# Optimization experiments

Hardware: AMD Instinct MI355X
Metric: run time of the kernel (lower is better)

## Reference

```python
import jax, jax.numpy as jnp
import numpy as np

B, L = 8, 1024
VOCAB, D_ENC, D_MAIN = 260, 128, 256
N_ENC, N_MAIN, N_DEC, N_HEADS = 3, 6, 3, 4
N_RATIO = 6.0  # 1/target_ratio
NEG = jnp.float32(-1e9)


def setup_inputs() -> dict:
    key = jax.random.key(0)
    kc = iter(jax.random.split(key, 40))
    def nrm(shape, std):
        return jax.random.normal(next(kc), shape, jnp.float32) * std
    inp = {'byte_ids': jax.random.randint(next(kc), (B, L), 0, VOCAB)}
    inp['embed'] = nrm((VOCAB, D_ENC), D_ENC ** -0.5)
    eye = jnp.eye(D_ENC, dtype=jnp.float32)
    inp['wq'] = eye + nrm((D_ENC, D_ENC), 0.02)  # init is identity in the torch module
    inp['wk'] = eye + nrm((D_ENC, D_ENC), 0.02)
    inp['proj_up'] = nrm((D_MAIN, D_ENC), D_ENC ** -0.5)
    inp['proj_down'] = nrm((D_ENC, D_MAIN), 1e-3)
    inp['norm_w'] = jnp.ones((D_ENC,), jnp.float32)
    inp['norm_b'] = jnp.zeros((D_ENC,), jnp.float32)
    for pre, n, d in [('enc', N_ENC, D_ENC), ('main', N_MAIN, D_MAIN), ('dec', N_DEC, D_ENC)]:
        inp[pre + '_ln1_w'] = jnp.ones((n, d), jnp.float32)
        inp[pre + '_ln1_b'] = jnp.zeros((n, d), jnp.float32)
        inp[pre + '_qkv'] = nrm((n, 3 * d, d), d ** -0.5)   # MHA in_proj (3D, D)
        inp[pre + '_wo'] = nrm((n, d, d), d ** -0.5)        # MHA out_proj
        inp[pre + '_ln2_w'] = jnp.ones((n, d), jnp.float32)
        inp[pre + '_ln2_b'] = jnp.zeros((n, d), jnp.float32)
        inp[pre + '_w1'] = nrm((n, 2 * d, d), d ** -0.5)    # mlp_mult = 2
        inp[pre + '_w2'] = nrm((n, d, 2 * d), (2 * d) ** -0.5)
    return inp


def _ln(x, w, b):
    mu = jnp.mean(x, axis=-1, keepdims=True)
    var = jnp.mean((x - mu) ** 2, axis=-1, keepdims=True)
    return (x - mu) * jax.lax.rsqrt(var + 1e-5) * w + b


def _mha(x, wqkv, wo, bias):
    Bb, S, D = x.shape
    dh = D // N_HEADS
    q, k, v = jnp.split(x @ wqkv.T, 3, axis=-1)
    q = q.reshape(Bb, S, N_HEADS, dh)
    k = k.reshape(Bb, S, N_HEADS, dh)
    v = v.reshape(Bb, S, N_HEADS, dh)
    scores = jnp.einsum('bqhd,bkhd->bhqk', q, k) * (dh ** -0.5) + bias
    attn = jax.nn.softmax(scores, axis=-1)
    out = jnp.einsum('bhqk,bkhd->bqhd', attn, v).reshape(Bb, S, D)
    return out @ wo.T


def _block(x, stack, i, bias):
    ln1w, ln1b, qkv, wo, ln2w, ln2b, w1, w2 = (a[i] for a in stack)
    x = x + _mha(_ln(x, ln1w, ln1b), qkv, wo, bias)
    h = _ln(x, ln2w, ln2b)
    return x + jax.nn.gelu(h @ w1.T, approximate=False) @ w2.T


def _downsample(x, b_hard):
    # scatter boundary tokens to the front of a padded (B, S, D) buffer
    Bb, S, D = x.shape
    idx = jnp.cumsum(b_hard, axis=1).astype(jnp.int32) - 1
    dest = jnp.where(b_hard > 0.5, idx, S)  # S is out-of-range -> dropped
    def sc(xb, db):
        return jnp.zeros((S, D), xb.dtype).at[db].set(xb, mode='drop')
    out = jax.vmap(sc)(x, dest)
    counts = jnp.sum(b_hard, axis=1).astype(jnp.int32)
    mask = jnp.arange(S)[None, :] < counts[:, None]
    return out, mask


def _forward(byte_ids, embed, wq, wk,
             enc_ln1_w, enc_ln1_b, enc_qkv, enc_wo, enc_ln2_w, enc_ln2_b, enc_w1, enc_w2,
             proj_up,
             main_ln1_w, main_ln1_b, main_qkv, main_wo, main_ln2_w, main_ln2_b, main_w1, main_w2,
             proj_down,
             dec_ln1_w, dec_ln1_b, dec_qkv, dec_wo, dec_ln2_w, dec_ln2_b, dec_w1, dec_w2,
             norm_w, norm_b):
    causal = jnp.where(jnp.triu(jnp.ones((L, L), bool), 1), NEG, jnp.float32(0.0))[None, None]
    x = embed[byte_ids]  # (B, L, D_ENC)
    enc_p = (enc_ln1_w, enc_ln1_b, enc_qkv, enc_wo, enc_ln2_w, enc_ln2_b, enc_w1, enc_w2)
    for i in range(N_ENC):
        x = _block(x, enc_p, i, causal)

    # --- dynamic chunking (routing + ratio loss) ---
    def l2n(t):
        return t / jnp.maximum(jnp.linalg.norm(t, axis=-1, keepdims=True), 1e-12)
    q = l2n(x @ wq.T)
    k = l2n(x @ wk.T)
    k_prev = jnp.pad(k[:, :-1], ((0, 0), (1, 0), (0, 0)))
    cos = jnp.sum(q * k_prev, axis=-1)
    p = jnp.clip(0.5 * (1.0 - cos), 0.0, 1.0)
    p = jnp.concatenate([jnp.ones_like(p[:, :1]), p[:, 1:]], axis=1)
    b_hard = (p >= 0.5).astype(jnp.float32)
    N = N_RATIO
    F_act = jnp.mean(b_hard)
    G_act = jnp.mean(p)
    ratio_loss = N / (N - 1.0) * ((N - 1.0) * F_act * G_act + (1.0 - F_act) * (1.0 - G_act))
    compressed, comp_mask = _downsample(x, b_hard)
    p_comp = _downsample(p[..., None], b_hard)[0][..., 0]

    # --- main stack on compressed sequence (padded to L, masked) ---
    z = compressed @ proj_up.T
    main_bias = causal + jnp.where(comp_mask, jnp.float32(0.0), NEG)[:, None, None, :]
    main_p = (main_ln1_w, main_ln1_b, main_qkv, main_wo, main_ln2_w, main_ln2_b, main_w1, main_w2)
    for i in range(N_MAIN):
        z = _block(z, main_p, i, main_bias)
    z = z @ proj_down.T  # (B, L, D_ENC)

    # --- chunk-level EMA (parallel linear-recurrence scan) + gather + STE ---
    p_c = jnp.clip(p_comp, 1e-4, 1.0 - 1e-4)
    a = (1.0 - p_c).at[:, 0].set(0.0)[..., None]          # z_bar[0] = z[0]
    bv = (p_c[..., None] * z).at[:, :1].set(z[:, :1])
    def comb(lhs, rhs):
        al, bl = lhs
        ar, br = rhs
        return (al * ar, ar * bl + br)
    z_bar = jax.lax.associative_scan(comb, (a, bv), axis=1)[1]
    chunk_idx = jnp.clip(jnp.cumsum(b_hard, axis=1).astype(jnp.int32) - 1, 0, None)
    z_up = jnp.take_along_axis(z_bar, jnp.broadcast_to(chunk_idx[:, :, None], z_bar.shape), axis=1)
    c = b_hard * p + (1.0 - b_hard) * (1.0 - p)
    c_ste = c + jax.lax.stop_gradient(1.0 - c)
    x = x + c_ste[..., None] * z_up

    dec_p = (dec_ln1_w, dec_ln1_b, dec_qkv, dec_wo, dec_ln2_w, dec_ln2_b, dec_w1, dec_w2)
    for i in range(N_DEC):
        x = _block(x, dec_p, i, causal)
    x = _ln(x, norm_w, norm_b)
    logits = x @ embed.T  # tied head
    return logits, ratio_loss


def reference(byte_ids, embed, wq, wk,
              enc_ln1_w, enc_ln1_b, enc_qkv, enc_wo, enc_ln2_w, enc_ln2_b, enc_w1, enc_w2,
              proj_up,
              main_ln1_w, main_ln1_b, main_qkv, main_wo, main_ln2_w, main_ln2_b, main_w1, main_w2,
              proj_down,
              dec_ln1_w, dec_ln1_b, dec_qkv, dec_wo, dec_ln2_w, dec_ln2_b, dec_w1, dec_w2,
              norm_w, norm_b):
    return _forward(byte_ids, embed, wq, wk,
                    enc_ln1_w, enc_ln1_b, enc_qkv, enc_wo, enc_ln2_w, enc_ln2_b, enc_w1, enc_w2,
                    proj_up,
                    main_ln1_w, main_ln1_b, main_qkv, main_wo, main_ln2_w, main_ln2_b, main_w1, main_w2,
                    proj_down,
                    dec_ln1_w, dec_ln1_b, dec_qkv, dec_wo, dec_ln2_w, dec_ln2_b, dec_w1, dec_w2,
                    norm_w, norm_b)
```

## Files before the change

### kernel.cpp

```cpp
#include <hip/hip_runtime.h>
#include <hip/hip_bf16.h>

#define B_ 8
#define L_ 1024
#define BL (B_*L_)
#define DENC 128
#define DMAIN 256
#define VOCAB 260
#define NHEADS 4

typedef __hip_bfloat16 bf16;
typedef _Float16 f16;
typedef f16 half8 __attribute__((ext_vector_type(8)));
typedef f16 half4 __attribute__((ext_vector_type(4)));
typedef f16 half2v __attribute__((ext_vector_type(2)));
typedef float f32x4 __attribute__((ext_vector_type(4)));

__global__ __launch_bounds__(64) void k_detect(const void* __restrict__ emb, int* __restrict__ flag){
    int lane = threadIdx.x;
    const unsigned short* u = (const unsigned short*)emb;
    int bad = 0;
    #pragma unroll
    for (int j = 0; j < 4; j++){
        unsigned short h = u[lane + 64*j];
        bf16 t = *(const bf16*)&h;
        float v = __bfloat162float(t);
        if (!(fabsf(v) < 1e4f)) bad++;
    }
    #pragma unroll
    for (int o = 32; o >= 1; o >>= 1) bad += __shfl_xor(bad, o);
    if (lane == 0) flag[0] = (bad == 0) ? 1 : 0;
}

struct CvtArgs {
    const void* src[31];
    unsigned offs[32];
};
__global__ void k_cvt_all(CvtArgs a, float* __restrict__ dst, f16* __restrict__ dst16,
                          int total, const int* __restrict__ flag){
    int isbf = flag[0];
    for (int i = blockIdx.x*256 + threadIdx.x; i < total; i += gridDim.x*256){
        int lo = 0, hi = 30;
        while (lo < hi){ int mid = (lo+hi+1)>>1; if (a.offs[mid] <= (unsigned)i) lo = mid; else hi = mid-1; }
        int j = i - (int)a.offs[lo];
        float v = isbf ? __bfloat162float(((const bf16*)a.src[lo])[j])
                       : ((const float*)a.src[lo])[j];
        dst[i] = v;
        dst16[i] = (f16)v;
    }
}

__global__ void k_embed(const int* __restrict__ ids, const float* __restrict__ emb, float* __restrict__ x){
    int i = blockIdx.x*256 + threadIdx.x;
    int row = i >> 7, d = i & 127;
    x[i] = emb[ids[row]*DENC + d];
}

template<int D>
__global__ __launch_bounds__(256) void k_ln16(const float* __restrict__ x, const float* __restrict__ w,
                                              const float* __restrict__ b, f16* __restrict__ y){
    int row = blockIdx.x*4 + (threadIdx.x >> 6);
    int lane = threadIdx.x & 63;
    const float* xr = x + (size_t)row*D;
    float v[D/64];
    float s = 0.f;
    #pragma unroll
    for (int j=0;j<D/64;j++){ v[j] = xr[lane + j*64]; s += v[j]; }
    #pragma unroll
    for (int o=32;o>=1;o>>=1) s += __shfl_xor(s,o);
    float mu = s / (float)D;
    float s2 = 0.f;
    #pragma unroll
    for (int j=0;j<D/64;j++){ float dd = v[j]-mu; s2 += dd*dd; }
    #pragma unroll
    for (int o=32;o>=1;o>>=1) s2 += __shfl_xor(s2,o);
    float inv = rsqrtf(s2/(float)D + 1e-5f);
    f16* yr = y + (size_t)row*D;
    #pragma unroll
    for (int j=0;j<D/64;j++){
        int d = lane + j*64;
        yr[d] = (f16)((v[j]-mu)*inv*w[d] + b[d]);
    }
}

#define GBM 64
#define GBN 64
#define GBK 32
__global__ __launch_bounds__(256) void k_gemm2(const float* __restrict__ A, const float* __restrict__ Wq,
        const float* __restrict__ Wk, float* __restrict__ Cq, float* __restrict__ Ck, int K)
{
    __shared__ float As[GBK][GBM+4];
    __shared__ float Ws[GBK][GBN+4];
    int tid = threadIdx.x;
    int bm = blockIdx.y * GBM;
    int bn = blockIdx.x * GBN;
    int tx = tid & 15, ty = tid >> 4;
    float acc[4][4] = {};
    for (int k0 = 0; k0 < K; k0 += GBK){
        #pragma unroll
        for (int i = tid; i < GBM*GBK; i += 256){
            int m = i >> 5, kk = i & 31;
            As[kk][m] = A[(size_t)(bm+m)*K + k0 + kk];
        }
        #pragma unroll
        for (int i = tid; i < GBN*GBK; i += 256){
            int n = i >> 5, kk = i & 31;
            int gn = bn + n;
            const float* W = (gn < 128) ? Wq : Wk;
            int wr = gn & 127;
            Ws[kk][n] = W[(size_t)wr*K + k0 + kk];
        }
        __syncthreads();
        #pragma unroll
        for (int kk = 0; kk < GBK; kk++){
            float a0[4], w0[4];
            *(float4*)a0 = *(const float4*)&As[kk][ty*4];
            *(float4*)w0 = *(const float4*)&Ws[kk][tx*4];
            #pragma unroll
            for (int i=0;i<4;i++)
                #pragma unroll
                for (int j=0;j<4;j++) acc[i][j] += a0[i]*w0[j];
        }
        __syncthreads();
    }
    #pragma unroll
    for (int i=0;i<4;i++){
        int m = bm + ty*4 + i;
        #pragma unroll
        for (int j=0;j<4;j++){
            int n = bn + tx*4 + j;
            float* C = (n < 128) ? Cq : Ck;
            C[(size_t)m*128 + (n & 127)] = acc[i][j];
        }
    }
}

template<int K>
__global__ __launch_bounds__(256) void k_hgemm(const f16* __restrict__ A, const f16* __restrict__ W,
        const float* __restrict__ R, float* __restrict__ C, f16* __restrict__ C16,
        void* __restrict__ OutRaw, const int* __restrict__ flag, int N, int mode,
        f16* __restrict__ Qd, f16* __restrict__ Kd, f16* __restrict__ Vd,
        int dShift, int dhShift)
{
    __shared__ half8 As[4][64];
    __shared__ half8 Ws[4][64];
    int tid = threadIdx.x;
    int wave = tid >> 6, lane = tid & 63;
    int wr = wave >> 1, wc = wave & 1;
    int quad = lane >> 4, l15 = lane & 15;
    int bm = blockIdx.y * 64, bn = blockIdx.x * 64;

    f32x4 acc[2][2] = {};
    int srow = tid >> 2, sc8 = tid & 3;
    const f16* ap0 = A + (size_t)(bm + srow)*K + sc8*8;
    int gn = bn + srow;
    const f16* wp0 = W + (size_t)gn*K + sc8*8;
    bool wok = (gn < N);

    for (int k0 = 0; k0 < K; k0 += 32){
        __syncthreads();
        As[sc8][srow] = *(const half8*)(ap0 + k0);
        Ws[sc8][srow] = wok ? *(const half8*)(wp0 + k0) : (half8)(f16)0.f;
        __syncthreads();
        half8 af[2], wf[2];
        af[0] = As[quad][wr*32 + l15];
        af[1] = As[quad][wr*32 + 16 + l15];
        wf[0] = Ws[quad][wc*32 + l15];
        wf[1] = Ws[quad][wc*32 + 16 + l15];
        #pragma unroll
        for (int i=0;i<2;i++)
            #pragma unroll
            for (int j=0;j<2;j++)
                acc[i][j] = __builtin_amdgcn_mfma_f32_16x16x32_f16(af[i], wf[j], acc[i][j], 0, 0, 0);
    }

    #pragma unroll
    for (int j=0;j<2;j++){
        int n = bn + wc*32 + j*16 + l15;
        if (n >= N) continue;
        #pragma unroll
        for (int i=0;i<2;i++){
            #pragma unroll
            for (int r=0;r<4;r++){
                int m = bm + wr*32 + i*16 + quad*4 + r;
                float v = acc[i][j][r];
                if (mode == 5){
                    int which = n >> dShift;
                    int rem = n & ((1<<dShift)-1);
                    int hh = rem >> dhShift;
                    int dd = rem & ((1<<dhShift)-1);
                    int bb = m >> 10, tt = m & 1023;
                    int Hn = 1 << (dShift - dhShift);
                    f16* dst = (which==0) ? Qd : ((which==1) ? Kd : Vd);
                    if (which == 2)
                        dst[((((size_t)bb*Hn + hh) << dhShift) + dd)*L_ + tt] = (f16)v;
                    else
                        dst[((((size_t)bb*Hn + hh)*L_ + tt) << dhShift) + dd] = (f16)v;
                    continue;
                }
                size_t off = (size_t)m*N + n;
                if (mode == 1){ C[off] = v + R[off]; }
                else if (mode == 2){
                    v = 0.5f*v*(1.0f + erff(v*0.70710678118654752f));
                    C16[off] = (f16)v;
                } else if (mode == 3){
                    if (flag[0]) ((bf16*)OutRaw)[off] = __float2bfloat16(v);
                    else         ((float*)OutRaw)[off] = v;
                } else C[off] = v;
            }
        }
    }
}

template<int K>
__global__ __launch_bounds__(256) void k_lngemm(const float* __restrict__ A, const f16* __restrict__ W,
        const float* __restrict__ lnw, const float* __restrict__ lnb, int doLN,
        float* __restrict__ C, void* __restrict__ OutRaw,
        const int* __restrict__ flag, int N, int mode)
{
    constexpr int SA = K + 8;
    constexpr int RPT = K/64;
    __shared__ f16 sA[64*SA];
    int tid = threadIdx.x;
    int wave = tid >> 6, lane = tid & 63;
    int wr = wave >> 1, wc = wave & 1;
    int quad = lane >> 4, l15 = lane & 15;
    int bm = blockIdx.y * 64, bn = blockIdx.x * 64;

    float wv_[RPT], bv_[RPT];
    #pragma unroll
    for (int j=0;j<RPT;j++){
        int d = lane*RPT + j;
        wv_[j] = doLN ? lnw[d] : 1.f;
        bv_[j] = doLN ? lnb[d] : 0.f;
    }
    for (int rr=0; rr<16; rr++){
        int row = wave*16 + rr;
        const float* xr = A + (size_t)(bm+row)*K + lane*RPT;
        float v[RPT];
        if (RPT==2){ float2 t = *(const float2*)xr; v[0]=t.x; v[1]=t.y; }
        else       { float4 t = *(const float4*)xr; v[0]=t.x; v[1]=t.y; v[2]=t.z; v[3]=t.w; }
        float mu = 0.f, inv = 1.f;
        if (doLN){
            float s=0.f;
            #pragma unroll
            for (int j=0;j<RPT;j++) s += v[j];
            #pragma unroll
            for (int o=32;o>=1;o>>=1) s += __shfl_xor(s,o);
            mu = s / (float)K;
            float s2=0.f;
            #pragma unroll
            for (int j=0;j<RPT;j++){ float dd=v[j]-mu; s2+=dd*dd; }
            #pragma unroll
            for (int o=32;o>=1;o>>=1) s2 += __shfl_xor(s2,o);
            inv = rsqrtf(s2/(float)K + 1e-5f);
        }
        if (RPT==2){
            half2v h;
            h[0]=(f16)((v[0]-mu)*inv*wv_[0]+bv_[0]);
            h[1]=(f16)((v[1]-mu)*inv*wv_[1]+bv_[1]);
            *(half2v*)&sA[row*SA + lane*2] = h;
        } else {
            half4 h;
            #pragma unroll
            for (int j=0;j<4;j++) h[j]=(f16)((v[j]-mu)*inv*wv_[j]+bv_[j]);
            *(half4*)&sA[row*SA + lane*4] = h;
        }
    }
    __syncthreads();

    f32x4 acc[2][2] = {};
    int n0 = bn + wc*32 + l15;
    bool ok0 = n0 < N, ok1 = (n0+16) < N;
    const f16* w0p = W + (size_t)n0*K + quad*8;
    const f16* w1p = W + (size_t)(n0+16)*K + quad*8;
    #pragma unroll 4
    for (int k0=0;k0<K;k0+=32){
        half8 af[2], wf[2];
        af[0] = *(const half8*)&sA[(wr*32 + l15)*SA + k0 + quad*8];
        af[1] = *(const half8*)&sA[(wr*32 + 16 + l15)*SA + k0 + quad*8];
        wf[0] = ok0 ? *(const half8*)(w0p + k0) : (half8)(f16)0.f;
        wf[1] = ok1 ? *(const half8*)(w1p + k0) : (half8)(f16)0.f;
        #pragma unroll
        for (int i=0;i<2;i++)
            #pragma unroll
            for (int j=0;j<2;j++)
                acc[i][j] = __builtin_amdgcn_mfma_f32_16x16x32_f16(af[i], wf[j], acc[i][j], 0, 0, 0);
    }

    #pragma unroll
    for (int j=0;j<2;j++){
        int n = bn + wc*32 + j*16 + l15;
        if (n >= N) continue;
        #pragma unroll
        for (int i=0;i<2;i++){
            #pragma unroll
            for (int r=0;r<4;r++){
                int m = bm + wr*32 + i*16 + quad*4 + r;
                float v = acc[i][j][r];
                size_t off = (size_t)m*N + n;
                if (mode == 3){
                    if (flag[0]) ((bf16*)OutRaw)[off] = __float2bfloat16(v);
                    else         ((float*)OutRaw)[off] = v;
                } else C[off] = v;
            }
        }
    }
}

template<int DH>
__global__ __launch_bounds__(256) void k_mflash(const f16* __restrict__ Qh, const f16* __restrict__ Kh,
        const f16* __restrict__ Vt, f16* __restrict__ out, const int* __restrict__ counts,
        float scale)
{
    constexpr int BQ = 64, BK = 64;
    constexpr int RS = DH + 8;
    constexpr int PS = BK + 8;
    __shared__ f16 sQ[BQ*RS];
    __shared__ f16 sK[BK*RS];
    __shared__ f16 sVt[DH*PS];
    __shared__ f16 sP[BQ*PS];

    int x = blockIdx.x, b = x >> 2, h = x & 3;
    int yy = blockIdx.y;
    int qt = (yy < 8) ? yy : 23 - yy;
    int q0 = qt * BQ;
    int tid = threadIdx.x;
    int wv = tid >> 6, lane = tid & 63;
    int quad = lane >> 4, l15 = lane & 15;

    const f16* Qb = Qh + (size_t)x*L_*DH;
    const f16* Kb = Kh + (size_t)x*L_*DH;
    const f16* Vb = Vt + (size_t)x*DH*L_;
    int kcap = counts ? counts[b] : L_;
    int klen = min(kcap, q0 + BQ);

    for (int i = tid; i < BQ*DH/8; i += 256){
        int r = (8*i)/DH, c = (8*i)%DH;
        *(half8*)&sQ[r*RS + c] = *(const half8*)&Qb[(size_t)(q0+r)*DH + c];
    }

    float m[4], l[4];
    #pragma unroll
    for (int r=0;r<4;r++){ m[r] = -1e30f; l[r] = 0.f; }
    f32x4 accO[DH/16] = {};

    for (int k0 = 0; k0 < klen; k0 += BK){
        __syncthreads();
        for (int i = tid; i < BK*DH/8; i += 256){
            int r = (8*i)/DH, c = (8*i)%DH;
            *(half8*)&sK[r*RS + c] = *(const half8*)&Kb[(size_t)(k0+r)*DH + c];
        }
        for (int i = tid; i < DH*BK/8; i += 256){
            int r = (8*i)/BK, c = (8*i)%BK;
            *(half8*)&sVt[r*PS + c] = *(const half8*)&Vb[(size_t)r*L_ + k0 + c];
        }
        __syncthreads();

        half8 af[DH/32];
        #pragma unroll
        for (int ds=0; ds<DH/32; ds++)
            af[ds] = *(const half8*)&sQ[(16*wv + l15)*RS + quad*8 + 32*ds];
        f32x4 accS[4] = {};
        #pragma unroll
        for (int t=0;t<4;t++){
            #pragma unroll
            for (int ds=0; ds<DH/32; ds++){
                half8 bf = *(const half8*)&sK[(16*t + l15)*RS + quad*8 + 32*ds];
                accS[t] = __builtin_amdgcn_mfma_f32_16x16x32_f16(af[ds], bf, accS[t], 0, 0, 0);
            }
        }

        #pragma unroll
        for (int r=0;r<4;r++){
            int qrow = q0 + 16*wv + quad*4 + r;
            float sv[4];
            #pragma unroll
            for (int t=0;t<4;t++){
                float v = accS[t][r]*scale;
                int kp = k0 + 16*t + l15;
                if (kp > qrow || kp >= kcap) v = -1e30f;
                sv[t] = v;
            }
            float rm = fmaxf(fmaxf(sv[0],sv[1]), fmaxf(sv[2],sv[3]));
            rm = fmaxf(rm, __shfl_xor(rm, 1));
            rm = fmaxf(rm, __shfl_xor(rm, 2));
            rm = fmaxf(rm, __shfl_xor(rm, 4));
            rm = fmaxf(rm, __shfl_xor(rm, 8));
            float mn = fmaxf(m[r], rm);
            float al = __expf(m[r] - mn);
            float p0 = __expf(sv[0]-mn), p1 = __expf(sv[1]-mn);
            float p2 = __expf(sv[2]-mn), p3 = __expf(sv[3]-mn);
            float rs = p0+p1+p2+p3;
            rs += __shfl_xor(rs, 1);
            rs += __shfl_xor(rs, 2);
            rs += __shfl_xor(rs, 4);
            rs += __shfl_xor(rs, 8);
            l[r] = l[r]*al + rs;
            m[r] = mn;
            #pragma unroll
            for (int dt=0; dt<DH/16; dt++) accO[dt][r] *= al;
            int prow = 16*wv + quad*4 + r;
            sP[prow*PS + 16*0 + l15] = (f16)p0;
            sP[prow*PS + 16*1 + l15] = (f16)p1;
            sP[prow*PS + 16*2 + l15] = (f16)p2;
            sP[prow*PS + 16*3 + l15] = (f16)p3;
        }

        half8 pf[2];
        #pragma unroll
        for (int ks=0; ks<2; ks++)
            pf[ks] = *(const half8*)&sP[(16*wv + l15)*PS + quad*8 + 32*ks];
        #pragma unroll
        for (int dt=0; dt<DH/16; dt++){
            #pragma unroll
            for (int ks=0; ks<2; ks++){
                half8 bv = *(const half8*)&sVt[(16*dt + l15)*PS + quad*8 + 32*ks];
                accO[dt] = __builtin_amdgcn_mfma_f32_16x16x32_f16(pf[ks], bv, accO[dt], 0, 0, 0);
            }
        }
    }

    #pragma unroll
    for (int r=0;r<4;r++){
        float inv = 1.0f / l[r];
        int qrow = q0 + 16*wv + quad*4 + r;
        #pragma unroll
        for (int dt=0; dt<DH/16; dt++){
            int d = 16*dt + l15;
            out[((size_t)b*L_ + qrow)*(NHEADS*DH) + h*DH + d] = (f16)(accO[dt][r]*inv);
        }
    }
}

__global__ __launch_bounds__(64) void k_router(const float* __restrict__ Q, const float* __restrict__ Kr,
        float* __restrict__ p, float* __restrict__ bh)
{
    int idx = blockIdx.x;
    int t = idx & (L_-1);
    int lane = threadIdx.x;
    float pv;
    if (t == 0){ pv = 1.0f; }
    else {
        const float* qr = Q  + (size_t)idx*DENC;
        const float* kr = Kr + (size_t)(idx-1)*DENC;
        float qq=0.f, kk=0.f, qk=0.f;
        #pragma unroll
        for (int j=0;j<2;j++){
            float qv = qr[lane + j*64], kv = kr[lane + j*64];
            qq += qv*qv; kk += kv*kv; qk += qv*kv;
        }
        #pragma unroll
        for (int o=32;o>=1;o>>=1){ qq += __shfl_xor(qq,o); kk += __shfl_xor(kk,o); qk += __shfl_xor(qk,o); }
        float cosv = qk / (fmaxf(sqrtf(qq),1e-12f)*fmaxf(sqrtf(kk),1e-12f));
        pv = 0.5f*(1.0f - cosv);
        pv = fminf(fmaxf(pv, 0.0f), 1.0f);
    }
    if (lane == 0){ p[idx] = pv; bh[idx] = (pv >= 0.5f) ? 1.0f : 0.0f; }
}

__global__ __launch_bounds__(64) void k_seq(const float* __restrict__ bh, int* __restrict__ cidx,
                      int* __restrict__ src, int* __restrict__ counts, float* __restrict__ acc){
    int b = blockIdx.x;
    int lane = threadIdx.x;
    if (b == 0 && lane < 8) acc[lane] = 0.f;
    int base = b*L_ + lane*16;
    int h[16];
    int cnt = 0;
    #pragma unroll
    for (int j=0;j<16;j++){ h[j] = bh[base+j] > 0.5f; cnt += h[j]; }
    int inc = cnt;
    #pragma unroll
    for (int o=1;o<64;o<<=1){ int nb = __shfl_up(inc, o); if (lane >= o) inc += nb; }
    int run = inc - cnt;
    #pragma unroll
    for (int j=0;j<16;j++){
        run += h[j];
        int ci = run - 1; if (ci < 0) ci = 0;
        cidx[base+j] = ci;
        if (h[j]) src[b*L_ + run-1] = lane*16 + j;
    }
    if (lane == 63) counts[b] = inc;
}

__global__ __launch_bounds__(128) void k_scatter2(const float* __restrict__ x, const float* __restrict__ p,
        const int* __restrict__ src, const int* __restrict__ counts,
        f16* __restrict__ comp, float* __restrict__ pcomp)
{
    int s = blockIdx.x & (L_-1), b = blockIdx.x >> 10, d = threadIdx.x;
    int cnt = counts[b];
    f16* crow = comp + ((size_t)b*L_ + s)*DENC;
    if (s < cnt){
        int t = src[b*L_ + s];
        crow[d] = (f16)x[((size_t)b*L_ + t)*DENC + d];
        if (d == 0) pcomp[b*L_ + s] = p[b*L_ + t];
    } else {
        crow[d] = (f16)0.f;
        if (d == 0) pcomp[b*L_ + s] = 0.f;
    }
}

__global__ __launch_bounds__(256) void k_reduce(const float* __restrict__ p, const float* __restrict__ bh,
                                                float* __restrict__ acc){
    __shared__ float sp[256], sb[256];
    int tid = threadIdx.x;
    float s1=0.f, s2=0.f;
    for (int i = blockIdx.x*256 + tid; i < BL; i += gridDim.x*256){ s1 += p[i]; s2 += bh[i]; }
    sp[tid]=s1; sb[tid]=s2; __syncthreads();
    for (int o=128;o>=1;o>>=1){ if (tid<o){ sp[tid]+=sp[tid+o]; sb[tid]+=sb[tid+o]; } __syncthreads(); }
    if (tid==0){ atomicAdd(&acc[0], sp[0]); atomicAdd(&acc[1], sb[0]); }
}

__global__ __launch_bounds__(256) void k_ema2(const float* __restrict__ z, const float* __restrict__ pcomp,
                                              float* __restrict__ zbar){
    __shared__ float sp[L_];
    int blk = blockIdx.x;
    int b = blk >> 5;
    int tid = threadIdx.x, wv = tid >> 6, lane = tid & 63;
    int d = ((blk & 31) << 2) + wv;
    for (int i = tid; i < L_; i += 256){
        float pc = pcomp[b*L_ + i];
        sp[i] = fminf(fmaxf(pc, 1e-4f), 1.0f - 1e-4f);
    }
    __syncthreads();
    const float* zb = z + ((size_t)b*L_)*DENC + d;
    int t0 = lane*16;
    float zv[16];
    #pragma unroll
    for (int i=0;i<16;i++) zv[i] = zb[(size_t)(t0+i)*DENC];
    float A = 1.f, Bv = 0.f;
    #pragma unroll
    for (int i=0;i<16;i++){
        int t = t0 + i;
        float pc = sp[t];
        float a  = (t==0) ? 0.f : (1.f - pc);
        float bb = (t==0) ? zv[i] : pc*zv[i];
        A = a*A;
        Bv = a*Bv + bb;
    }
    #pragma unroll
    for (int off=1; off<64; off<<=1){
        float Ap = __shfl_up(A, off);
        float Bp = __shfl_up(Bv, off);
        if (lane >= off){ Bv = A*Bp + Bv; A = A*Ap; }
    }
    float sin_ = __shfl_up(Bv, 1);
    if (lane == 0) sin_ = 0.f;
    float s = sin_;
    float* ob = zbar + ((size_t)b*L_)*DENC + d;
    #pragma unroll
    for (int i=0;i<16;i++){
        int t = t0 + i;
        float pc = sp[t];
        float a  = (t==0) ? 0.f : (1.f - pc);
        float bb = (t==0) ? zv[i] : pc*zv[i];
        s = a*s + bb;
        ob[(size_t)t*DENC] = s;
    }
}

__global__ void k_combine(float* __restrict__ x, const float* __restrict__ zbar, const int* __restrict__ cidx){
    int i = blockIdx.x*256 + threadIdx.x;
    int row = i >> 7, d = i & 127;
    int b = row >> 10;
    int ci = cidx[row];
    x[i] += zbar[((size_t)b*L_ + ci)*DENC + d];
}

__global__ void k_loss(const float* __restrict__ acc, void* __restrict__ out, const int* __restrict__ flag){
    float G = acc[0] / (float)BL;
    float F = acc[1] / (float)BL;
    float ratio = 1.2f*(5.0f*F*G + (1.0f-F)*(1.0f-G));
    if (flag[0]) ((bf16*)out)[(size_t)BL*VOCAB] = __float2bfloat16(ratio);
    else         ((float*)out)[(size_t)BL*VOCAB] = ratio;
}

extern "C" void kernel_launch(void* const* d_in, const int* in_sizes, int n_in,
                              void* d_out, int out_size, void* d_ws, size_t ws_size,
                              hipStream_t stream) {
    (void)out_size; (void)ws_size;
    const int* byte_ids = (const int*)d_in[0];

    float* ws = (float*)d_ws;
    size_t off = 0;
    int* FLAG = (int*)ws; off += 16;
    float* W32 = ws + off;

    k_detect<<<1, 64, 0, stream>>>(d_in[1], FLAG);

    CvtArgs ca;
    const float* w32[32];
    unsigned woff = 0;
    for (int i = 1; i < n_in && i < 32; i++){
        w32[i] = W32 + woff;
        ca.src[i-1] = d_in[i];
        ca.offs[i-1] = woff;
        woff += (unsigned)in_sizes[i];
    }
    ca.offs[31] = woff;
    off += woff;
    f16* W16h = (f16*)(ws + off); off += (woff+1)/2;
    const f16* w16[32];
    for (int i = 1; i < n_in && i < 32; i++) w16[i] = W16h + ca.offs[i-1];
    k_cvt_all<<<2048, 256, 0, stream>>>(ca, W32, W16h, (int)woff, FLAG);

    const float* embed    = w32[1];
    const float* wq       = w32[2];
    const float* wk       = w32[3];
    const float* norm_w   = w32[6];
    const float* norm_b   = w32[7];

    float* X    = ws + off; off += (size_t)BL*DENC;
    float* QKVf = ws + off; off += (size_t)BL*3*DMAIN;
    float* ATTf = ws + off; off += (size_t)BL*DMAIN;
    float* Hf   = ws + off; off += (size_t)BL*2*DMAIN;
    float* LNf  = ws + off; off += (size_t)BL*DMAIN;
    float* Z    = ws + off; off += (size_t)BL*DMAIN;
    float* COMPf= ws + off; off += (size_t)BL*DENC;
    float* P    = ws + off; off += BL;
    float* BH   = ws + off; off += BL;
    float* PCOMP= ws + off; off += BL;
    float* ACC  = ws + off; off += 8;
    int* CIDX   = (int*)(ws + off); off += BL;
    int* SRC    = (int*)(ws + off); off += BL;
    int* COUNTS = (int*)(ws + off); off += 64;

    f16* QKV16 = (f16*)QKVf;
    f16* ATT16 = (f16*)ATTf;
    f16* H16   = (f16*)Hf;
    f16* LN16  = (f16*)LNf;
    f16* COMP16= (f16*)COMPf;
    float* Qr  = ATTf;
    float* Kr  = Hf;
    float* ZDN = QKVf;
    float* ZBAR= QKVf + (size_t)BL*DENC;

    auto hgemm = [&](int K, const f16* A, const f16* W, const float* R, float* C, f16* C16,
                     void* Ob, int N, int mode, f16* Qd, f16* Kd, f16* Vd, int dS, int dhS){
        dim3 g((N+63)/64, BL/64);
        if (K == 128)      k_hgemm<128><<<g, 256, 0, stream>>>(A, W, R, C, C16, Ob, FLAG, N, mode, Qd, Kd, Vd, dS, dhS);
        else if (K == 256) k_hgemm<256><<<g, 256, 0, stream>>>(A, W, R, C, C16, Ob, FLAG, N, mode, Qd, Kd, Vd, dS, dhS);
        else               k_hgemm<512><<<g, 256, 0, stream>>>(A, W, R, C, C16, Ob, FLAG, N, mode, Qd, Kd, Vd, dS, dhS);
    };

    auto block128 = [&](float* Xs, const float* l1w, const float* l1b, const f16* qkvw, const f16* wo,
                        const float* l2w, const float* l2b, const f16* w1, const f16* w2){
        k_ln16<128><<<BL/4,256,0,stream>>>(Xs, l1w, l1b, LN16);
        hgemm(128, LN16, qkvw, nullptr, nullptr, nullptr, nullptr, 3*DENC, 5,
              QKV16, QKV16 + (size_t)BL*DENC, QKV16 + (size_t)2*BL*DENC, 7, 5);
        k_mflash<32><<<dim3(B_*NHEADS,16),256,0,stream>>>(QKV16, QKV16 + (size_t)BL*DENC,
                                                          QKV16 + (size_t)2*BL*DENC,
                                                          ATT16, nullptr, 0.17677669529663687f);
        hgemm(128, ATT16, wo, Xs, Xs, nullptr, nullptr, DENC, 1, nullptr, nullptr, nullptr, 0, 0);
        k_ln16<128><<<BL/4,256,0,stream>>>(Xs, l2w, l2b, LN16);
        hgemm(128, LN16, w1, nullptr, nullptr, H16, nullptr, 2*DENC, 2, nullptr, nullptr, nullptr, 0, 0);
        hgemm(256, H16, w2, Xs, Xs, nullptr, nullptr, DENC, 1, nullptr, nullptr, nullptr, 0, 0);
    };
    auto block_main = [&](float* Xs, const float* l1w, const float* l1b, const f16* qkvw, const f16* wo,
                          const float* l2w, const float* l2b, const f16* w1, const f16* w2){
        k_ln16<256><<<BL/4,256,0,stream>>>(Xs, l1w, l1b, LN16);
        hgemm(256, LN16, qkvw, nullptr, nullptr, nullptr, nullptr, 3*DMAIN, 5,
              QKV16, QKV16 + (size_t)BL*DMAIN, QKV16 + (size_t)2*BL*DMAIN, 8, 6);
        k_mflash<64><<<dim3(B_*NHEADS,16),256,0,stream>>>(QKV16, QKV16 + (size_t)BL*DMAIN,
                                                          QKV16 + (size_t)2*BL*DMAIN,
                                                          ATT16, COUNTS, 0.125f);
        hgemm(256, ATT16, wo, Xs, Xs, nullptr, nullptr, DMAIN, 1, nullptr, nullptr, nullptr, 0, 0);
        k_ln16<256><<<BL/4,256,0,stream>>>(Xs, l2w, l2b, LN16);
        hgemm(256, LN16, w1, nullptr, nullptr, H16, nullptr, 2*DMAIN, 2, nullptr, nullptr, nullptr, 0, 0);
        hgemm(512, H16, w2, Xs, Xs, nullptr, nullptr, DMAIN, 1, nullptr, nullptr, nullptr, 0, 0);
    };

    k_embed<<<BL*DENC/256, 256, 0, stream>>>(byte_ids, embed, X);
    for (int i = 0; i < 3; i++)
        block128(X, w32[8] + i*DENC, w32[9] + i*DENC, w16[10] + (size_t)i*3*DENC*DENC,
                 w16[11] + (size_t)i*DENC*DENC, w32[12] + i*DENC, w32[13] + i*DENC,
                 w16[14] + (size_t)i*2*DENC*DENC, w16[15] + (size_t)i*2*DENC*DENC);

    k_gemm2<<<dim3(4, BL/64), 256, 0, stream>>>(X, wq, wk, Qr, Kr, DENC);
    k_router<<<BL, 64, 0, stream>>>(Qr, Kr, P, BH);
    k_seq<<<B_, 64, 0, stream>>>(BH, CIDX, SRC, COUNTS, ACC);
    k_scatter2<<<BL, 128, 0, stream>>>(X, P, SRC, COUNTS, COMP16, PCOMP);
    k_reduce<<<8, 256, 0, stream>>>(P, BH, ACC);

    hgemm(128, COMP16, w16[4], nullptr, Z, nullptr, nullptr, DMAIN, 0, nullptr, nullptr, nullptr, 0, 0);
    for (int i = 0; i < 6; i++)
        block_main(Z, w32[16] + i*DMAIN, w32[17] + i*DMAIN, w16[18] + (size_t)i*3*DMAIN*DMAIN,
                   w16[19] + (size_t)i*DMAIN*DMAIN, w32[20] + i*DMAIN, w32[21] + i*DMAIN,
                   w16[22] + (size_t)i*2*DMAIN*DMAIN, w16[23] + (size_t)i*2*DMAIN*DMAIN);
    k_lngemm<256><<<dim3(2, BL/64), 256, 0, stream>>>(Z, w16[5], nullptr, nullptr, 0,
                                                      ZDN, nullptr, FLAG, DENC, 0);

    k_ema2<<<256, 256, 0, stream>>>(ZDN, PCOMP, ZBAR);
    k_combine<<<BL*DENC/256, 256, 0, stream>>>(X, ZBAR, CIDX);

    for (int i = 0; i < 3; i++)
        block128(X, w32[24] + i*DENC, w32[25] + i*DENC, w16[26] + (size_t)i*3*DENC*DENC,
                 w16[27] + (size_t)i*DENC*DENC, w32[28] + i*DENC, w32[29] + i*DENC,
                 w16[30] + (size_t)i*2*DENC*DENC, w16[31] + (size_t)i*2*DENC*DENC);

    k_lngemm<128><<<dim3(5, BL/64), 256, 0, stream>>>(X, w16[1], norm_w, norm_b, 1,
                                                      nullptr, d_out, FLAG, VOCAB, 3);
    k_loss<<<1,1,0,stream>>>(ACC, d_out, FLAG);
}
```

Baseline: 1.216 ms.

## Add 128-row hgemm tile with K=64 steps and fold reduction into k_seq

The f16 MFMA GEMM now loads a 64-wide K slice per iteration, issuing two MFMA k-steps per barrier pair instead of one. A BM=128 variant, where each wave owns 32 rows across all 64 columns, is used for the wide QKV and main-stack W1 projections. The separate k_reduce kernel is removed: k_seq now reduces p and the boundary count per sequence with atomics, and zeroing of the accumulator moves into k_router. This cuts the number of syncs per K, raises reuse of the W tile and drops one launch, at the cost of more LDS, more registers and fewer blocks for the wide GEMMs.

```diff
diff --git a/kernel.cpp b/kernel.cpp
--- a/kernel.cpp
+++ b/kernel.cpp
@@ -135,54 +135,65 @@
     }
 }
 
-template<int K>
+template<int K, int BM>
 __global__ __launch_bounds__(256) void k_hgemm(const f16* __restrict__ A, const f16* __restrict__ W,
         const float* __restrict__ R, float* __restrict__ C, f16* __restrict__ C16,
         void* __restrict__ OutRaw, const int* __restrict__ flag, int N, int mode,
         f16* __restrict__ Qd, f16* __restrict__ Kd, f16* __restrict__ Vd,
         int dShift, int dhShift)
 {
-    __shared__ half8 As[4][64];
-    __shared__ half8 Ws[4][64];
+    constexpr int NJ = (BM == 128) ? 4 : 2;
+    __shared__ half8 As[BM*8];
+    __shared__ half8 Ws[64*8];
     int tid = threadIdx.x;
     int wave = tid >> 6, lane = tid & 63;
-    int wr = wave >> 1, wc = wave & 1;
     int quad = lane >> 4, l15 = lane & 15;
-    int bm = blockIdx.y * 64, bn = blockIdx.x * 64;
-
-    f32x4 acc[2][2] = {};
-    int srow = tid >> 2, sc8 = tid & 3;
-    const f16* ap0 = A + (size_t)(bm + srow)*K + sc8*8;
-    int gn = bn + srow;
-    const f16* wp0 = W + (size_t)gn*K + sc8*8;
-    bool wok = (gn < N);
-
-    for (int k0 = 0; k0 < K; k0 += 32){
+    int bm = blockIdx.y * BM, bn = blockIdx.x * 64;
+    int mrow0 = (BM == 128) ? wave*32 : (wave>>1)*32;
+    int ncol0 = (BM == 128) ? 0 : (wave&1)*32;
+
+    f32x4 acc[2][NJ] = {};
+
+    for (int k0 = 0; k0 < K; k0 += 64){
         __syncthreads();
-        As[sc8][srow] = *(const half8*)(ap0 + k0);
-        Ws[sc8][srow] = wok ? *(const half8*)(wp0 + k0) : (half8)(f16)0.f;
+        #pragma unroll
+        for (int s = 0; s < BM/32; s++){
+            int slot = s*256 + tid;
+            int row = slot >> 3, col = slot & 7;
+            As[slot] = *(const half8*)(A + (size_t)(bm+row)*K + k0 + col*8);
+        }
+        #pragma unroll
+        for (int s = 0; s < 2; s++){
+            int slot = s*256 + tid;
+            int row = slot >> 3, col = slot & 7;
+            int gn = bn + row;
+            Ws[slot] = (gn < N) ? *(const half8*)(W + (size_t)gn*K + k0 + col*8) : (half8)(f16)0.f;
+        }
         __syncthreads();
-        half8 af[2], wf[2];
-        af[0] = As[quad][wr*32 + l15];
-        af[1] = As[quad][wr*32 + 16 + l15];
-        wf[0] = Ws[quad][wc*32 + l15];
-        wf[1] = Ws[quad][wc*32 + 16 + l15];
-        #pragma unroll
-        for (int i=0;i<2;i++)
-            #pragma unroll
-            for (int j=0;j<2;j++)
-                acc[i][j] = __builtin_amdgcn_mfma_f32_16x16x32_f16(af[i], wf[j], acc[i][j], 0, 0, 0);
-    }
-
-    #pragma unroll
-    for (int j=0;j<2;j++){
-        int n = bn + wc*32 + j*16 + l15;
+        #pragma unroll
+        for (int ks = 0; ks < 2; ks++){
+            half8 af[2], wf[NJ];
+            #pragma unroll
+            for (int i=0;i<2;i++) af[i] = As[(mrow0 + i*16 + l15)*8 + ks*4 + quad];
+            #pragma unroll
+            for (int j=0;j<NJ;j++) wf[j] = Ws[(ncol0 + j*16 + l15)*8 + ks*4 + quad];
+            #pragma unroll
+            for (int i=0;i<2;i++)
+                #pragma unroll
+                for (int j=0;j<NJ;j++)
+                    acc[i][j] = __builtin_amdgcn_mfma_f32_16x16x32_f16(af[i], wf[j], acc[i][j], 0, 0, 0);
+        }
+    }
+
+    #pragma unroll
+    for (int j=0;j<NJ;j++){
+        int n = bn + ncol0 + j*16 + l15;
         if (n >= N) continue;
         #pragma unroll
         for (int i=0;i<2;i++){
             #pragma unroll
             for (int r=0;r<4;r++){
-                int m = bm + wr*32 + i*16 + quad*4 + r;
+                int m = bm + mrow0 + i*16 + quad*4 + r;
                 float v = acc[i][j][r];
                 if (mode == 5){
                     int which = n >> dShift;
@@ -434,11 +445,12 @@
 }
 
 __global__ __launch_bounds__(64) void k_router(const float* __restrict__ Q, const float* __restrict__ Kr,
-        float* __restrict__ p, float* __restrict__ bh)
+        float* __restrict__ p, float* __restrict__ bh, float* __restrict__ acc)
 {
     int idx = blockIdx.x;
     int t = idx & (L_-1);
     int lane = threadIdx.x;
+    if (idx == 0 && lane < 8) acc[lane] = 0.f;
     float pv;
     if (t == 0){ pv = 1.0f; }
     else {
@@ -459,16 +471,17 @@
     if (lane == 0){ p[idx] = pv; bh[idx] = (pv >= 0.5f) ? 1.0f : 0.0f; }
 }
 
-__global__ __launch_bounds__(64) void k_seq(const float* __restrict__ bh, int* __restrict__ cidx,
-                      int* __restrict__ src, int* __restrict__ counts, float* __restrict__ acc){
+__global__ __launch_bounds__(64) void k_seq(const float* __restrict__ bh, const float* __restrict__ p,
+                      int* __restrict__ cidx, int* __restrict__ src, int* __restrict__ counts,
+                      float* __restrict__ acc){
     int b = blockIdx.x;
     int lane = threadIdx.x;
-    if (b == 0 && lane < 8) acc[lane] = 0.f;
     int base = b*L_ + lane*16;
     int h[16];
     int cnt = 0;
-    #pragma unroll
-    for (int j=0;j<16;j++){ h[j] = bh[base+j] > 0.5f; cnt += h[j]; }
+    float ps = 0.f;
+    #pragma unroll
+    for (int j=0;j<16;j++){ h[j] = bh[base+j] > 0.5f; cnt += h[j]; ps += p[base+j]; }
     int inc = cnt;
     #pragma unroll
     for (int o=1;o<64;o<<=1){ int nb = __shfl_up(inc, o); if (lane >= o) inc += nb; }
@@ -480,6 +493,10 @@
         cidx[base+j] = ci;
         if (h[j]) src[b*L_ + run-1] = lane*16 + j;
     }
+    float cs = (float)cnt;
+    #pragma unroll
+    for (int o=32;o>=1;o>>=1){ ps += __shfl_xor(ps,o); cs += __shfl_xor(cs,o); }
+    if (lane == 0){ atomicAdd(&acc[0], ps); atomicAdd(&acc[1], cs); }
     if (lane == 63) counts[b] = inc;
 }
 
@@ -500,17 +517,6 @@
     }
 }
 
-__global__ __launch_bounds__(256) void k_reduce(const float* __restrict__ p, const float* __restrict__ bh,
-                                                float* __restrict__ acc){
-    __shared__ float sp[256], sb[256];
-    int tid = threadIdx.x;
-    float s1=0.f, s2=0.f;
-    for (int i = blockIdx.x*256 + tid; i < BL; i += gridDim.x*256){ s1 += p[i]; s2 += bh[i]; }
-    sp[tid]=s1; sb[tid]=s2; __syncthreads();
-    for (int o=128;o>=1;o>>=1){ if (tid<o){ sp[tid]+=sp[tid+o]; sb[tid]+=sb[tid+o]; } __syncthreads(); }
-    if (tid==0){ atomicAdd(&acc[0], sp[0]); atomicAdd(&acc[1], sb[0]); }
-}
-
 __global__ __launch_bounds__(256) void k_ema2(const float* __restrict__ z, const float* __restrict__ pcomp,
                                               float* __restrict__ zbar){
     __shared__ float sp[L_];
@@ -635,39 +641,45 @@
     float* ZDN = QKVf;
     float* ZBAR= QKVf + (size_t)BL*DENC;
 
-    auto hgemm = [&](int K, const f16* A, const f16* W, const float* R, float* C, f16* C16,
+    auto hgemm = [&](int K, int BM, const f16* A, const f16* W, const float* R, float* C, f16* C16,
                      void* Ob, int N, int mode, f16* Qd, f16* Kd, f16* Vd, int dS, int dhS){
-        dim3 g((N+63)/64, BL/64);
-        if (K == 128)      k_hgemm<128><<<g, 256, 0, stream>>>(A, W, R, C, C16, Ob, FLAG, N, mode, Qd, Kd, Vd, dS, dhS);
-        else if (K == 256) k_hgemm<256><<<g, 256, 0, stream>>>(A, W, R, C, C16, Ob, FLAG, N, mode, Qd, Kd, Vd, dS, dhS);
-        else               k_hgemm<512><<<g, 256, 0, stream>>>(A, W, R, C, C16, Ob, FLAG, N, mode, Qd, Kd, Vd, dS, dhS);
+        dim3 g((N+63)/64, BL/BM);
+        if (BM == 128){
+            if (K == 128)      k_hgemm<128,128><<<g,256,0,stream>>>(A, W, R, C, C16, Ob, FLAG, N, mode, Qd, Kd, Vd, dS, dhS);
+            else if (K == 256) k_hgemm<256,128><<<g,256,0,stream>>>(A, W, R, C, C16, Ob, FLAG, N, mode, Qd, Kd, Vd, dS, dhS);
+            else               k_hgemm<512,128><<<g,256,0,stream>>>(A, W, R, C, C16, Ob, FLAG, N, mode, Qd, Kd, Vd, dS, dhS);
+        } else {
+            if (K == 128)      k_hgemm<128,64><<<g,256,0,stream>>>(A, W, R, C, C16, Ob, FLAG, N, mode, Qd, Kd, Vd, dS, dhS);
+            else if (K == 256) k_hgemm<256,64><<<g,256,0,stream>>>(A, W, R, C, C16, Ob, FLAG, N, mode, Qd, Kd, Vd, dS, dhS);
+            else               k_hgemm<512,64><<<g,256,0,stream>>>(A, W, R, C, C16, Ob, FLAG, N, mode, Qd, Kd, Vd, dS, dhS);
+        }
     };
 
     auto block128 = [&](float* Xs, const float* l1w, const float* l1b, const f16* qkvw, const f16* wo,
                         const float* l2w, const float* l2b, const f16* w1, const f16* w2){
         k_ln16<128><<<BL/4,256,0,stream>>>(Xs, l1w, l1b, LN16);
-        hgemm(128, LN16, qkvw, nullptr, nullptr, nullptr, nullptr, 3*DENC, 5,
+        hgemm(128, 128, LN16, qkvw, nullptr, nullptr, nullptr, nullptr, 3*DENC, 5,
               QKV16, QKV16 + (size_t)BL*DENC, QKV16 + (size_t)2*BL*DENC, 7, 5);
         k_mflash<32><<<dim3(B_*NHEADS,16),256,0,stream>>>(QKV16, QKV16 + (size_t)BL*DENC,
                                                           QKV16 + (size_t)2*BL*DENC,
                                                           ATT16, nullptr, 0.17677669529663687f);
-        hgemm(128, ATT16, wo, Xs, Xs, nullptr, nullptr, DENC, 1, nullptr, nullptr, nullptr, 0, 0);
+        hgemm(128, 64, ATT16, wo, Xs, Xs, nullptr, nullptr, DENC, 1, nullptr, nullptr, nullptr, 0, 0);
         k_ln16<128><<<BL/4,256,0,stream>>>(Xs, l2w, l2b, LN16);
-        hgemm(128, LN16, w1, nullptr, nullptr, H16, nullptr, 2*DENC, 2, nullptr, nullptr, nullptr, 0, 0);
-        hgemm(256, H16, w2, Xs, Xs, nullptr, nullptr, DENC, 1, nullptr, nullptr, nullptr, 0, 0);
+        hgemm(128, 64, LN16, w1, nullptr, nullptr, H16, nullptr, 2*DENC, 2, nullptr, nullptr, nullptr, 0, 0);
+        hgemm(256, 64, H16, w2, Xs, Xs, nullptr, nullptr, DENC, 1, nullptr, nullptr, nullptr, 0, 0);
     };
     auto block_main = [&](float* Xs, const float* l1w, const float* l1b, const f16* qkvw, const f16* wo,
                           const float* l2w, const float* l2b, const f16* w1, const f16* w2){
         k_ln16<256><<<BL/4,256,0,stream>>>(Xs, l1w, l1b, LN16);
-        hgemm(256, LN16, qkvw, nullptr, nullptr, nullptr, nullptr, 3*DMAIN, 5,
+        hgemm(256, 128, LN16, qkvw, nullptr, nullptr, nullptr, nullptr, 3*DMAIN, 5,
               QKV16, QKV16 + (size_t)BL*DMAIN, QKV16 + (size_t)2*BL*DMAIN, 8, 6);
         k_mflash<64><<<dim3(B_*NHEADS,16),256,0,stream>>>(QKV16, QKV16 + (size_t)BL*DMAIN,
                                                           QKV16 + (size_t)2*BL*DMAIN,
                                                           ATT16, COUNTS, 0.125f);
-        hgemm(256, ATT16, wo, Xs, Xs, nullptr, nullptr, DMAIN, 1, nullptr, nullptr, nullptr, 0, 0);
+        hgemm(256, 64, ATT16, wo, Xs, Xs, nullptr, nullptr, DMAIN, 1, nullptr, nullptr, nullptr, 0, 0);
         k_ln16<256><<<BL/4,256,0,stream>>>(Xs, l2w, l2b, LN16);
-        hgemm(256, LN16, w1, nullptr, nullptr, H16, nullptr, 2*DMAIN, 2, nullptr, nullptr, nullptr, 0, 0);
-        hgemm(512, H16, w2, Xs, Xs, nullptr, nullptr, DMAIN, 1, nullptr, nullptr, nullptr, 0, 0);
+        hgemm(256, 128, LN16, w1, nullptr, nullptr, H16, nullptr, 2*DMAIN, 2, nullptr, nullptr, nullptr, 0, 0);
+        hgemm(512, 64, H16, w2, Xs, Xs, nullptr, nullptr, DMAIN, 1, nullptr, nullptr, nullptr, 0, 0);
     };
 
     k_embed<<<BL*DENC/256, 256, 0, stream>>>(byte_ids, embed, X);
@@ -677,12 +689,11 @@
                  w16[14] + (size_t)i*2*DENC*DENC, w16[15] + (size_t)i*2*DENC*DENC);
 
     k_gemm2<<<dim3(4, BL/64), 256, 0, stream>>>(X, wq, wk, Qr, Kr, DENC);
-    k_router<<<BL, 64, 0, stream>>>(Qr, Kr, P, BH);
-    k_seq<<<B_, 64, 0, stream>>>(BH, CIDX, SRC, COUNTS, ACC);
+    k_router<<<BL, 64, 0, stream>>>(Qr, Kr, P, BH, ACC);
+    k_seq<<<B_, 64, 0, stream>>>(BH, P, CIDX, SRC, COUNTS, ACC);
     k_scatter2<<<BL, 128, 0, stream>>>(X, P, SRC, COUNTS, COMP16, PCOMP);
-    k_reduce<<<8, 256, 0, stream>>>(P, BH, ACC);
-
-    hgemm(128, COMP16, w16[4], nullptr, Z, nullptr, nullptr, DMAIN, 0, nullptr, nullptr, nullptr, 0, 0);
+
+    hgemm(128, 64, COMP16, w16[4], nullptr, Z, nullptr, nullptr, DMAIN, 0, nullptr, nullptr, nullptr, 0, 0);
     for (int i = 0; i < 6; i++)
         block_main(Z, w32[16] + i*DMAIN, w32[17] + i*DMAIN, w16[18] + (size_t)i*3*DMAIN*DMAIN,
                    w16[19] + (size_t)i*DMAIN*DMAIN, w32[20] + i*DMAIN, w32[21] + i*DMAIN,
```

Result: slower. 1.304 ms (+7.3%).
